# Optimization experiments

Hardware: AMD Instinct MI355X
Metric: run time of the kernel (lower is better)

The kernel has to match this reference:

```python
import jax, jax.numpy as jnp
import numpy as np

N = 100000
E = 1600000
IN, HID, OUT = 128, 256, 128


def setup_inputs() -> dict:
    key = jax.random.key(0)
    ks = jax.random.split(key, 8)
    x = jax.random.normal(ks[0], (N, IN), dtype=jnp.float32)
    edge_index = jax.random.randint(ks[1], (2, E), 0, N, dtype=jnp.int64)
    # PyG SAGEConv params: lin_l (neighbor aggr, with bias), lin_r (root, no bias)
    def glorot(k, shape):
        fan_in = shape[1]
        return jax.random.normal(k, shape, dtype=jnp.float32) / jnp.sqrt(jnp.float32(fan_in))
    W1l = glorot(ks[2], (HID, IN)); b1 = jnp.zeros((HID,), jnp.float32)
    W1r = glorot(ks[3], (HID, IN))
    W2l = glorot(ks[4], (OUT, HID)); b2 = jnp.zeros((OUT,), jnp.float32)
    W2r = glorot(ks[5], (OUT, HID))
    return {"x": x, "edge_index": edge_index, "W1l": W1l, "b1": b1,
            "W1r": W1r, "W2l": W2l, "b2": b2, "W2r": W2r}


def sage_conv(x, row, col, Wl, b, Wr, n_nodes):
    # mean-aggregate neighbor features x[row] at target nodes col
    msg = x[row]                                               # [E, d]
    s = jax.ops.segment_sum(msg, col, num_segments=n_nodes)    # [N, d]
    deg = jax.ops.segment_sum(jnp.ones((row.shape[0], 1), x.dtype), col,
                              num_segments=n_nodes)            # [N, 1]
    mean = s / jnp.maximum(deg, 1.0)
    return mean @ Wl.T + b + x @ Wr.T


def reference(x, edge_index, W1l, b1, W1r, W2l, b2, W2r):
    row, col = edge_index[0], edge_index[1]
    h = sage_conv(x, row, col, W1l, b1, W1r, N)
    h = jax.nn.relu(h)
    # dropout is identity in eval mode
    out = sage_conv(h, row, col, W2l, b2, W2r, N)
    return out
```

## Files before the change

kernel.cpp:

```cpp
#include <hip/hip_runtime.h>
#include <hip/hip_bf16.h>

#define NN 100000
#define NE 1600000
#define NCHUNK ((NN + 127) / 128)
#define NPB 512
#define NB 256
#define CHUNK 8192
#define NCH ((NE + CHUNK - 1) / CHUNK)

typedef __attribute__((ext_vector_type(8))) short short8;
typedef __attribute__((ext_vector_type(4))) float float4v;

__device__ __forceinline__ unsigned short f2bf(float f) {
    unsigned int b = __float_as_uint(f);
    return (unsigned short)((b + 0x7fffu + ((b >> 16) & 1u)) >> 16);
}
__device__ __forceinline__ unsigned int pack_bf16(float lo, float hi) {
    return (unsigned int)f2bf(lo) | ((unsigned int)f2bf(hi) << 16);
}
__device__ __forceinline__ float bflo(unsigned int u) { return __uint_as_float(u << 16); }
__device__ __forceinline__ float bfhi(unsigned int u) { return __uint_as_float(u & 0xffff0000u); }

__device__ __forceinline__ void addp(float* a, uint4 u) {
    a[0] += bflo(u.x); a[1] += bfhi(u.x);
    a[2] += bflo(u.y); a[3] += bfhi(u.y);
    a[4] += bflo(u.z); a[5] += bfhi(u.z);
    a[6] += bflo(u.w); a[7] += bfhi(u.w);
}

__global__ void k_wconv(const float* W1l, const float* W1r, const float* W2l, const float* W2r,
                        unsigned short* wb1, unsigned short* wb2) {
    int i = blockIdx.x * 256 + threadIdx.x;
    int r1 = i >> 7, c1 = i & 127;
    wb1[r1 * 256 + c1]       = f2bf(W1l[i]);
    wb1[r1 * 256 + 128 + c1] = f2bf(W1r[i]);
    wb2[i]         = f2bf(W2l[i]);
    wb2[32768 + i] = f2bf(W2r[i]);
}

__global__ void k_xconv(const float* x, unsigned int* axb_u) {
    int t = blockIdx.x * 256 + threadIdx.x;
    int node = t >> 6, i = t & 63;
    float2 v = ((const float2*)x)[t];
    axb_u[(size_t)node * 128 + 64 + i] = pack_bf16(v.x, v.y);
}

__global__ void k_bcount(const int* ei, int* bcnt) {
    __shared__ int h[NB];
    int t = threadIdx.x;
    h[t] = 0;
    __syncthreads();
    for (int e = blockIdx.x * 256 + t; e < NE; e += gridDim.x * 256)
        atomicAdd(&h[ei[NE + e] >> 9], 1);
    __syncthreads();
    if (h[t]) atomicAdd(&bcnt[t], h[t]);
}

__global__ void k_bscan(const int* bcnt, int* boff, int* bcur) {
    __shared__ int s[NB];
    int t = threadIdx.x;
    int v = bcnt[t];
    s[t] = v;
    __syncthreads();
    for (int d = 1; d < NB; d <<= 1) {
        int val = (t >= d) ? s[t - d] : 0;
        __syncthreads();
        s[t] += val;
        __syncthreads();
    }
    boff[t + 1] = s[t];
    if (t == 0) boff[0] = 0;
    bcur[t] = s[t] - v;
}

__global__ __launch_bounds__(256) void k_bscatter(const int* ei, int* bcur, uint2* pairs) {
    __shared__ uint2 buf[CHUNK];
    __shared__ int cnt[NB];
    __shared__ int lbase[NB];
    __shared__ int lcur[NB];
    __shared__ int gpos[NB];
    int t = threadIdx.x;
    int e0 = blockIdx.x * CHUNK;
    int nedge = NE - e0; if (nedge > CHUNK) nedge = CHUNK;
    cnt[t] = 0;
    __syncthreads();
    for (int i = t; i < nedge; i += 256)
        atomicAdd(&cnt[ei[NE + e0 + i] >> 9], 1);
    __syncthreads();
    int v = cnt[t];
    lcur[t] = v;
    __syncthreads();
    for (int d = 1; d < NB; d <<= 1) {
        int val = (t >= d) ? lcur[t - d] : 0;
        __syncthreads();
        lcur[t] += val;
        __syncthreads();
    }
    lbase[t] = lcur[t] - v;
    gpos[t] = atomicAdd(&bcur[t], v);
    __syncthreads();
    lcur[t] = lbase[t];
    __syncthreads();
    for (int i = t; i < nedge; i += 256) {
        int r = ei[e0 + i], c = ei[NE + e0 + i];
        int b = c >> 9;
        int p = atomicAdd(&lcur[b], 1);
        buf[p] = make_uint2((unsigned)r, (unsigned)c);
    }
    __syncthreads();
    int n = cnt[t], lb = lbase[t], gp = gpos[t];
    for (int i = 0; i < n; i++)
        pairs[gp + i] = buf[lb + i];
}

__global__ __launch_bounds__(256) void k_build(const uint2* pairs, const int* boff,
                                               int* off, int* deg, int* csr) {
    __shared__ int ldeg[NPB];
    __shared__ int lcur[NPB];
    __shared__ int sscan[256];
    int b = blockIdx.x;
    int nbase = b * NPB;
    if (nbase >= NN) return;
    int t = threadIdx.x;
    int base = boff[b], cntb = boff[b + 1] - base;
    ldeg[t] = 0; ldeg[t + 256] = 0;
    __syncthreads();
    for (int i = t; i < cntb; i += 256) {
        uint2 pr = pairs[base + i];
        atomicAdd(&ldeg[pr.y - nbase], 1);
    }
    __syncthreads();
    int d0 = ldeg[2 * t], d1 = ldeg[2 * t + 1];
    int v = d0 + d1;
    sscan[t] = v;
    __syncthreads();
    for (int d = 1; d < 256; d <<= 1) {
        int val = (t >= d) ? sscan[t - d] : 0;
        __syncthreads();
        sscan[t] += val;
        __syncthreads();
    }
    int ex = sscan[t] - v;
    lcur[2 * t] = ex; lcur[2 * t + 1] = ex + d0;
    __syncthreads();
    int nloc = NN - nbase; if (nloc > NPB) nloc = NPB;
    for (int ln = t; ln < nloc; ln += 256) {
        off[nbase + ln] = base + lcur[ln];
        deg[nbase + ln] = ldeg[ln];
    }
    __syncthreads();
    for (int i = t; i < cntb; i += 256) {
        uint2 pr = pairs[base + i];
        int p = atomicAdd(&lcur[pr.y - nbase], 1);
        csr[base + p] = (int)pr.x;
    }
}

__global__ void k_agg1(const unsigned int* axb_u, const int* off, const int* deg,
                       const int* csr, unsigned int* axb_w) {
    int wid = (blockIdx.x * 256 + threadIdx.x) >> 6;
    if (wid >= NN) return;
    int lane = threadIdx.x & 63;
    int sub = lane >> 4, l16 = lane & 15;
    int start = off[wid], d = deg[wid];
    float a[8] = {0.f, 0.f, 0.f, 0.f, 0.f, 0.f, 0.f, 0.f};
    int j = sub;
    for (; j + 4 < d; j += 8) {
        int nb0 = csr[start + j];
        int nb1 = csr[start + j + 4];
        uint4 u0 = *(const uint4*)(axb_u + (size_t)nb0 * 128 + 64 + (l16 << 2));
        uint4 u1 = *(const uint4*)(axb_u + (size_t)nb1 * 128 + 64 + (l16 << 2));
        addp(a, u0); addp(a, u1);
    }
    if (j < d) {
        int nb = csr[start + j];
        uint4 u = *(const uint4*)(axb_u + (size_t)nb * 128 + 64 + (l16 << 2));
        addp(a, u);
    }
#pragma unroll
    for (int i = 0; i < 8; i++) {
        a[i] += __shfl_xor(a[i], 16, 64);
        a[i] += __shfl_xor(a[i], 32, 64);
    }
    if (sub == 0) {
        float inv = 1.0f / (float)(d > 0 ? d : 1);
        uint4 o;
        o.x = pack_bf16(a[0] * inv, a[1] * inv);
        o.y = pack_bf16(a[2] * inv, a[3] * inv);
        o.z = pack_bf16(a[4] * inv, a[5] * inv);
        o.w = pack_bf16(a[6] * inv, a[7] * inv);
        *(uint4*)(axb_w + (size_t)wid * 128 + (l16 << 2)) = o;
    }
}

__global__ void k_agg2(const unsigned int* g, const int* off, const int* deg,
                       const int* csr, float* out) {
    int wid = (blockIdx.x * 256 + threadIdx.x) >> 6;
    if (wid >= NN) return;
    int lane = threadIdx.x & 63;
    int sub = lane >> 4, l16 = lane & 15;
    int start = off[wid], d = deg[wid];
    float a[8] = {0.f, 0.f, 0.f, 0.f, 0.f, 0.f, 0.f, 0.f};
    int j = sub;
    for (; j + 4 < d; j += 8) {
        int nb0 = csr[start + j];
        int nb1 = csr[start + j + 4];
        uint4 u0 = *(const uint4*)(g + (size_t)nb0 * 64 + (l16 << 2));
        uint4 u1 = *(const uint4*)(g + (size_t)nb1 * 64 + (l16 << 2));
        addp(a, u0); addp(a, u1);
    }
    if (j < d) {
        int nb = csr[start + j];
        uint4 u = *(const uint4*)(g + (size_t)nb * 64 + (l16 << 2));
        addp(a, u);
    }
#pragma unroll
    for (int i = 0; i < 8; i++) {
        a[i] += __shfl_xor(a[i], 16, 64);
        a[i] += __shfl_xor(a[i], 32, 64);
    }
    if (sub == 0) {
        float inv = 1.0f / (float)(d > 0 ? d : 1);
        float4* po = (float4*)(out + (size_t)wid * 128) + (l16 << 1);
        float4 c0 = po[0], c1 = po[1];
        c0.x += a[0] * inv; c0.y += a[1] * inv; c0.z += a[2] * inv; c0.w += a[3] * inv;
        c1.x += a[4] * inv; c1.y += a[5] * inv; c1.z += a[6] * inv; c1.w += a[7] * inv;
        po[0] = c0; po[1] = c1;
    }
}

__global__ __launch_bounds__(256, 1) void k_gemm1(const unsigned short* A, const unsigned short* wb,
                                                  const float* b1, unsigned short* H) {
    __shared__ unsigned short Bs[256 * 256];
    int t = threadIdx.x;
    {
        const short8* src = (const short8*)wb;
        short8* dst = (short8*)Bs;
#pragma unroll
        for (int i = 0; i < 32; i++) dst[i * 256 + t] = src[i * 256 + t];
    }
    __syncthreads();
    int wv = t >> 6, lane = t & 63;
    int mrow = lane & 15, quad = lane >> 4;
    float bias[16];
#pragma unroll
    for (int ct = 0; ct < 16; ct++) bias[ct] = b1[ct * 16 + mrow];
    for (int chunk = blockIdx.x; chunk < NCHUNK; chunk += gridDim.x) {
        int base = chunk * 128 + wv * 32;
        if (base >= NN) continue;
        short8 afr[2][8];
#pragma unroll
        for (int kk = 0; kk < 8; kk++) {
            afr[0][kk] = *(const short8*)(A + (size_t)(base + mrow) * 256 + kk * 32 + quad * 8);
            afr[1][kk] = *(const short8*)(A + (size_t)(base + 16 + mrow) * 256 + kk * 32 + quad * 8);
        }
        float4v acc[2][16];
#pragma unroll
        for (int h = 0; h < 2; h++)
#pragma unroll
            for (int ct = 0; ct < 16; ct++) acc[h][ct] = (float4v)(0.0f);
#pragma unroll
        for (int kk = 0; kk < 8; kk++) {
            int koff = kk * 32 + quad * 8;
#pragma unroll
            for (int ct = 0; ct < 16; ct++) {
                short8 b = *(const short8*)(Bs + (ct * 16 + mrow) * 256 + koff);
                acc[0][ct] = __builtin_amdgcn_mfma_f32_16x16x32_bf16(afr[0][kk], b, acc[0][ct], 0, 0, 0);
                acc[1][ct] = __builtin_amdgcn_mfma_f32_16x16x32_bf16(afr[1][kk], b, acc[1][ct], 0, 0, 0);
            }
        }
#pragma unroll
        for (int ct = 0; ct < 16; ct++) {
            int col = ct * 16 + mrow;
#pragma unroll
            for (int h = 0; h < 2; h++) {
#pragma unroll
                for (int r = 0; r < 4; r++) {
                    int node = base + h * 16 + quad * 4 + r;
                    float v = acc[h][ct][r] + bias[ct];
                    v = fmaxf(v, 0.f);
                    H[(size_t)node * 256 + col] = f2bf(v);
                }
            }
        }
    }
}

__global__ __launch_bounds__(256, 1) void k_gemm2(const unsigned short* A, const unsigned short* wb,
                                                  const float* b2, unsigned short* g, float* out) {
    __shared__ unsigned short Bs[256 * 256];
    int t = threadIdx.x;
    {
        const short8* src = (const short8*)wb;
        short8* dst = (short8*)Bs;
#pragma unroll
        for (int i = 0; i < 32; i++) dst[i * 256 + t] = src[i * 256 + t];
    }
    __syncthreads();
    int wv = t >> 6, lane = t & 63;
    int mrow = lane & 15, quad = lane >> 4;
    float bias[8];
#pragma unroll
    for (int i = 0; i < 8; i++) bias[i] = b2[i * 16 + mrow];
    for (int chunk = blockIdx.x; chunk < NCHUNK; chunk += gridDim.x) {
        int base = chunk * 128 + wv * 32;
        if (base >= NN) continue;
        short8 afr[2][8];
#pragma unroll
        for (int kk = 0; kk < 8; kk++) {
            afr[0][kk] = *(const short8*)(A + (size_t)(base + mrow) * 256 + kk * 32 + quad * 8);
            afr[1][kk] = *(const short8*)(A + (size_t)(base + 16 + mrow) * 256 + kk * 32 + quad * 8);
        }
        float4v acc[2][16];
#pragma unroll
        for (int h = 0; h < 2; h++)
#pragma unroll
            for (int ct = 0; ct < 16; ct++) acc[h][ct] = (float4v)(0.0f);
#pragma unroll
        for (int kk = 0; kk < 8; kk++) {
            int koff = kk * 32 + quad * 8;
#pragma unroll
            for (int ct = 0; ct < 16; ct++) {
                short8 b = *(const short8*)(Bs + (ct * 16 + mrow) * 256 + koff);
                acc[0][ct] = __builtin_amdgcn_mfma_f32_16x16x32_bf16(afr[0][kk], b, acc[0][ct], 0, 0, 0);
                acc[1][ct] = __builtin_amdgcn_mfma_f32_16x16x32_bf16(afr[1][kk], b, acc[1][ct], 0, 0, 0);
            }
        }
#pragma unroll
        for (int ct = 0; ct < 16; ct++) {
            int col = ct * 16 + mrow;
#pragma unroll
            for (int h = 0; h < 2; h++) {
#pragma unroll
                for (int r = 0; r < 4; r++) {
                    int node = base + h * 16 + quad * 4 + r;
                    float v = acc[h][ct][r];
                    if (ct < 8) {
                        g[(size_t)node * 128 + col] = f2bf(v);
                    } else {
                        out[(size_t)node * 128 + (col - 128)] = v + bias[ct - 8];
                    }
                }
            }
        }
    }
}

extern "C" void kernel_launch(void* const* d_in, const int* in_sizes, int n_in,
                              void* d_out, int out_size, void* d_ws, size_t ws_size,
                              hipStream_t stream) {
    const float* x   = (const float*)d_in[0];
    const int*   ei  = (const int*)d_in[1];
    const float* W1l = (const float*)d_in[2];
    const float* b1  = (const float*)d_in[3];
    const float* W1r = (const float*)d_in[4];
    const float* W2l = (const float*)d_in[5];
    const float* b2  = (const float*)d_in[6];
    const float* W2r = (const float*)d_in[7];
    float* out = (float*)d_out;

    char* p = (char*)d_ws;
    unsigned int* axb = (unsigned int*)p; p += (size_t)NN * 256 * 2;
    unsigned short* h = (unsigned short*)p; p += (size_t)NN * 256 * 2;
    unsigned int* g   = (unsigned int*)p;  p += (size_t)NN * 128 * 2;
    unsigned short* wb1 = (unsigned short*)p; p += 65536 * 2;
    unsigned short* wb2 = (unsigned short*)p; p += 65536 * 2;
    int* deg  = (int*)p; p += (size_t)NN * 4;
    int* off  = (int*)p; p += (size_t)NN * 4;
    int* csr  = (int*)p; p += (size_t)NE * 4;
    int* bcnt = (int*)p; p += NB * 4;
    int* boff = (int*)p; p += (NB + 1) * 4;
    int* bcur = (int*)p; p += NB * 4;
    if (ws_size < (size_t)(p - (char*)d_ws)) return;
    uint2* pairs = (uint2*)h;

    hipMemsetAsync(bcnt, 0, NB * 4, stream);
    k_wconv<<<128, 256, 0, stream>>>(W1l, W1r, W2l, W2r, wb1, wb2);
    k_xconv<<<NN * 64 / 256, 256, 0, stream>>>(x, axb);
    k_bcount<<<256, 256, 0, stream>>>(ei, bcnt);
    k_bscan<<<1, NB, 0, stream>>>(bcnt, boff, bcur);
    k_bscatter<<<NCH, 256, 0, stream>>>(ei, bcur, pairs);
    k_build<<<NB, 256, 0, stream>>>(pairs, boff, off, deg, csr);
    k_agg1<<<NN * 64 / 256, 256, 0, stream>>>(axb, off, deg, csr, axb);
    k_gemm1<<<256, 256, 0, stream>>>((const unsigned short*)axb, wb1, b1, h);
    k_gemm2<<<256, 256, 0, stream>>>(h, wb2, b2, (unsigned short*)g, out);
    k_agg2<<<25000, 256, 0, stream>>>(g, off, deg, csr, out);
}
```

Baseline: 396.5 us.

## Merge prep kernels, unroll gather loops, and double-buffer A fragments in GEMMs

Merges the weight conversion, x conversion and bucket-count kernels into one launch that splits work by block index, which removes two launches. Widens the neighbor-gather loops in both aggregation kernels to keep four loads in flight per lane group. Makes both GEMM kernels prefetch the next chunk's A fragments into a second register buffer while the current chunk runs its MFMAs. The extra buffer doubles A-fragment register use and may add spills, and the bcount edge partition of 256×6250 relies on E being exactly 1.6M.

After: 410.4 us. 1.03x slower.

```diff
diff --git a/kernel.cpp b/kernel.cpp
--- a/kernel.cpp
+++ b/kernel.cpp
@@ -29,32 +29,33 @@
     a[6] += bflo(u.w); a[7] += bfhi(u.w);
 }
 
-__global__ void k_wconv(const float* W1l, const float* W1r, const float* W2l, const float* W2r,
-                        unsigned short* wb1, unsigned short* wb2) {
-    int i = blockIdx.x * 256 + threadIdx.x;
-    int r1 = i >> 7, c1 = i & 127;
-    wb1[r1 * 256 + c1]       = f2bf(W1l[i]);
-    wb1[r1 * 256 + 128 + c1] = f2bf(W1r[i]);
-    wb2[i]         = f2bf(W2l[i]);
-    wb2[32768 + i] = f2bf(W2r[i]);
-}
-
-__global__ void k_xconv(const float* x, unsigned int* axb_u) {
-    int t = blockIdx.x * 256 + threadIdx.x;
-    int node = t >> 6, i = t & 63;
-    float2 v = ((const float2*)x)[t];
-    axb_u[(size_t)node * 128 + 64 + i] = pack_bf16(v.x, v.y);
-}
-
-__global__ void k_bcount(const int* ei, int* bcnt) {
-    __shared__ int h[NB];
-    int t = threadIdx.x;
-    h[t] = 0;
-    __syncthreads();
-    for (int e = blockIdx.x * 256 + t; e < NE; e += gridDim.x * 256)
-        atomicAdd(&h[ei[NE + e] >> 9], 1);
-    __syncthreads();
-    if (h[t]) atomicAdd(&bcnt[t], h[t]);
+__global__ void k_prep(const float* x, const float* W1l, const float* W1r,
+                       const float* W2l, const float* W2r, const int* ei,
+                       unsigned int* axb_u, unsigned short* wb1, unsigned short* wb2,
+                       int* bcnt) {
+    __shared__ int hh[NB];
+    int b = blockIdx.x, t = threadIdx.x;
+    if (b < 25000) {
+        int tt = b * 256 + t;
+        int node = tt >> 6, i = tt & 63;
+        float2 v = ((const float2*)x)[tt];
+        axb_u[(size_t)node * 128 + 64 + i] = pack_bf16(v.x, v.y);
+    } else if (b < 25128) {
+        int i = (b - 25000) * 256 + t;
+        int r1 = i >> 7, c1 = i & 127;
+        wb1[r1 * 256 + c1]       = f2bf(W1l[i]);
+        wb1[r1 * 256 + 128 + c1] = f2bf(W1r[i]);
+        wb2[i]         = f2bf(W2l[i]);
+        wb2[32768 + i] = f2bf(W2r[i]);
+    } else {
+        hh[t] = 0;
+        __syncthreads();
+        int e0 = (b - 25128) * 6250;
+        for (int e = e0 + t; e < e0 + 6250; e += 256)
+            atomicAdd(&hh[ei[NE + e] >> 9], 1);
+        __syncthreads();
+        if (hh[t]) atomicAdd(&bcnt[t], hh[t]);
+    }
 }
 
 __global__ void k_bscan(const int* bcnt, int* boff, int* bcur) {
@@ -164,18 +165,23 @@
     int lane = threadIdx.x & 63;
     int sub = lane >> 4, l16 = lane & 15;
     int start = off[wid], d = deg[wid];
+    const unsigned int* gp = axb_u + 64 + (l16 << 2);
     float a[8] = {0.f, 0.f, 0.f, 0.f, 0.f, 0.f, 0.f, 0.f};
     int j = sub;
-    for (; j + 4 < d; j += 8) {
-        int nb0 = csr[start + j];
-        int nb1 = csr[start + j + 4];
-        uint4 u0 = *(const uint4*)(axb_u + (size_t)nb0 * 128 + 64 + (l16 << 2));
-        uint4 u1 = *(const uint4*)(axb_u + (size_t)nb1 * 128 + 64 + (l16 << 2));
-        addp(a, u0); addp(a, u1);
-    }
-    if (j < d) {
+    for (; j + 12 < d; j += 16) {
+        int n0 = csr[start + j];
+        int n1 = csr[start + j + 4];
+        int n2 = csr[start + j + 8];
+        int n3 = csr[start + j + 12];
+        uint4 u0 = *(const uint4*)(gp + (size_t)n0 * 128);
+        uint4 u1 = *(const uint4*)(gp + (size_t)n1 * 128);
+        uint4 u2 = *(const uint4*)(gp + (size_t)n2 * 128);
+        uint4 u3 = *(const uint4*)(gp + (size_t)n3 * 128);
+        addp(a, u0); addp(a, u1); addp(a, u2); addp(a, u3);
+    }
+    for (; j < d; j += 4) {
         int nb = csr[start + j];
-        uint4 u = *(const uint4*)(axb_u + (size_t)nb * 128 + 64 + (l16 << 2));
+        uint4 u = *(const uint4*)(gp + (size_t)nb * 128);
         addp(a, u);
     }
 #pragma unroll
@@ -201,18 +207,23 @@
     int lane = threadIdx.x & 63;
     int sub = lane >> 4, l16 = lane & 15;
     int start = off[wid], d = deg[wid];
+    const unsigned int* gp = g + (l16 << 2);
     float a[8] = {0.f, 0.f, 0.f, 0.f, 0.f, 0.f, 0.f, 0.f};
     int j = sub;
-    for (; j + 4 < d; j += 8) {
-        int nb0 = csr[start + j];
-        int nb1 = csr[start + j + 4];
-        uint4 u0 = *(const uint4*)(g + (size_t)nb0 * 64 + (l16 << 2));
-        uint4 u1 = *(const uint4*)(g + (size_t)nb1 * 64 + (l16 << 2));
-        addp(a, u0); addp(a, u1);
-    }
-    if (j < d) {
+    for (; j + 12 < d; j += 16) {
+        int n0 = csr[start + j];
+        int n1 = csr[start + j + 4];
+        int n2 = csr[start + j + 8];
+        int n3 = csr[start + j + 12];
+        uint4 u0 = *(const uint4*)(gp + (size_t)n0 * 64);
+        uint4 u1 = *(const uint4*)(gp + (size_t)n1 * 64);
+        uint4 u2 = *(const uint4*)(gp + (size_t)n2 * 64);
+        uint4 u3 = *(const uint4*)(gp + (size_t)n3 * 64);
+        addp(a, u0); addp(a, u1); addp(a, u2); addp(a, u3);
+    }
+    for (; j < d; j += 4) {
         int nb = csr[start + j];
-        uint4 u = *(const uint4*)(g + (size_t)nb * 64 + (l16 << 2));
+        uint4 u = *(const uint4*)(gp + (size_t)nb * 64);
         addp(a, u);
     }
 #pragma unroll
@@ -230,6 +241,32 @@
     }
 }
 
+__device__ __forceinline__ void loadA(short8 afr[2][8], const unsigned short* A,
+                                      int base, int mrow, int quad) {
+#pragma unroll
+    for (int kk = 0; kk < 8; kk++) {
+        afr[0][kk] = *(const short8*)(A + (size_t)(base + mrow) * 256 + kk * 32 + quad * 8);
+        afr[1][kk] = *(const short8*)(A + (size_t)(base + 16 + mrow) * 256 + kk * 32 + quad * 8);
+    }
+}
+__device__ __forceinline__ void mfmaAcc(float4v acc[2][16], short8 afr[2][8],
+                                        const unsigned short* Bs, int mrow, int quad) {
+#pragma unroll
+    for (int h = 0; h < 2; h++)
+#pragma unroll
+        for (int ct = 0; ct < 16; ct++) acc[h][ct] = (float4v)(0.0f);
+#pragma unroll
+    for (int kk = 0; kk < 8; kk++) {
+        int koff = kk * 32 + quad * 8;
+#pragma unroll
+        for (int ct = 0; ct < 16; ct++) {
+            short8 b = *(const short8*)(Bs + (ct * 16 + mrow) * 256 + koff);
+            acc[0][ct] = __builtin_amdgcn_mfma_f32_16x16x32_bf16(afr[0][kk], b, acc[0][ct], 0, 0, 0);
+            acc[1][ct] = __builtin_amdgcn_mfma_f32_16x16x32_bf16(afr[1][kk], b, acc[1][ct], 0, 0, 0);
+        }
+    }
+}
+
 __global__ __launch_bounds__(256, 1) void k_gemm1(const unsigned short* A, const unsigned short* wb,
                                                   const float* b1, unsigned short* H) {
     __shared__ unsigned short Bs[256 * 256];
@@ -240,50 +277,41 @@
 #pragma unroll
         for (int i = 0; i < 32; i++) dst[i * 256 + t] = src[i * 256 + t];
     }
-    __syncthreads();
     int wv = t >> 6, lane = t & 63;
     int mrow = lane & 15, quad = lane >> 4;
     float bias[16];
 #pragma unroll
     for (int ct = 0; ct < 16; ct++) bias[ct] = b1[ct * 16 + mrow];
-    for (int chunk = blockIdx.x; chunk < NCHUNK; chunk += gridDim.x) {
-        int base = chunk * 128 + wv * 32;
-        if (base >= NN) continue;
-        short8 afr[2][8];
-#pragma unroll
-        for (int kk = 0; kk < 8; kk++) {
-            afr[0][kk] = *(const short8*)(A + (size_t)(base + mrow) * 256 + kk * 32 + quad * 8);
-            afr[1][kk] = *(const short8*)(A + (size_t)(base + 16 + mrow) * 256 + kk * 32 + quad * 8);
+    short8 afrA[2][8], afrB[2][8];
+    int chunk = blockIdx.x;
+    int base = chunk * 128 + wv * 32;
+    if (base < NN) loadA(afrA, A, base, mrow, quad);
+    __syncthreads();
+    bool useA = true;
+    while (chunk < NCHUNK) {
+        int cn = chunk + 256;
+        int bn = cn * 128 + wv * 32;
+        if (cn < NCHUNK && bn < NN) {
+            if (useA) loadA(afrB, A, bn, mrow, quad);
+            else      loadA(afrA, A, bn, mrow, quad);
         }
-        float4v acc[2][16];
-#pragma unroll
-        for (int h = 0; h < 2; h++)
-#pragma unroll
-            for (int ct = 0; ct < 16; ct++) acc[h][ct] = (float4v)(0.0f);
-#pragma unroll
-        for (int kk = 0; kk < 8; kk++) {
-            int koff = kk * 32 + quad * 8;
+        if (base < NN) {
+            float4v acc[2][16];
+            mfmaAcc(acc, useA ? afrA : afrB, Bs, mrow, quad);
 #pragma unroll
             for (int ct = 0; ct < 16; ct++) {
-                short8 b = *(const short8*)(Bs + (ct * 16 + mrow) * 256 + koff);
-                acc[0][ct] = __builtin_amdgcn_mfma_f32_16x16x32_bf16(afr[0][kk], b, acc[0][ct], 0, 0, 0);
-                acc[1][ct] = __builtin_amdgcn_mfma_f32_16x16x32_bf16(afr[1][kk], b, acc[1][ct], 0, 0, 0);
+                int col = ct * 16 + mrow;
+#pragma unroll
+                for (int h = 0; h < 2; h++)
+#pragma unroll
+                    for (int r = 0; r < 4; r++) {
+                        int node = base + h * 16 + quad * 4 + r;
+                        float v = acc[h][ct][r] + bias[ct];
+                        H[(size_t)node * 256 + col] = f2bf(fmaxf(v, 0.f));
+                    }
             }
         }
-#pragma unroll
-        for (int ct = 0; ct < 16; ct++) {
-            int col = ct * 16 + mrow;
-#pragma unroll
-            for (int h = 0; h < 2; h++) {
-#pragma unroll
-                for (int r = 0; r < 4; r++) {
-                    int node = base + h * 16 + quad * 4 + r;
-                    float v = acc[h][ct][r] + bias[ct];
-                    v = fmaxf(v, 0.f);
-                    H[(size_t)node * 256 + col] = f2bf(v);
-                }
-            }
-        }
+        chunk = cn; base = bn; useA = !useA;
     }
 }
 
@@ -297,53 +325,42 @@
 #pragma unroll
         for (int i = 0; i < 32; i++) dst[i * 256 + t] = src[i * 256 + t];
     }
-    __syncthreads();
     int wv = t >> 6, lane = t & 63;
     int mrow = lane & 15, quad = lane >> 4;
     float bias[8];
 #pragma unroll
     for (int i = 0; i < 8; i++) bias[i] = b2[i * 16 + mrow];
-    for (int chunk = blockIdx.x; chunk < NCHUNK; chunk += gridDim.x) {
-        int base = chunk * 128 + wv * 32;
-        if (base >= NN) continue;
-        short8 afr[2][8];
-#pragma unroll
-        for (int kk = 0; kk < 8; kk++) {
-            afr[0][kk] = *(const short8*)(A + (size_t)(base + mrow) * 256 + kk * 32 + quad * 8);
-            afr[1][kk] = *(const short8*)(A + (size_t)(base + 16 + mrow) * 256 + kk * 32 + quad * 8);
+    short8 afrA[2][8], afrB[2][8];
+    int chunk = blockIdx.x;
+    int base = chunk * 128 + wv * 32;
+    if (base < NN) loadA(afrA, A, base, mrow, quad);
+    __syncthreads();
+    bool useA = true;
+    while (chunk < NCHUNK) {
+        int cn = chunk + 256;
+        int bn = cn * 128 + wv * 32;
+        if (cn < NCHUNK && bn < NN) {
+            if (useA) loadA(afrB, A, bn, mrow, quad);
+            else      loadA(afrA, A, bn, mrow, quad);
         }
-        float4v acc[2][16];
-#pragma unroll
-        for (int h = 0; h < 2; h++)
-#pragma unroll
-            for (int ct = 0; ct < 16; ct++) acc[h][ct] = (float4v)(0.0f);
-#pragma unroll
-        for (int kk = 0; kk < 8; kk++) {
-            int koff = kk * 32 + quad * 8;
+        if (base < NN) {
+            float4v acc[2][16];
+            mfmaAcc(acc, useA ? afrA : afrB, Bs, mrow, quad);
 #pragma unroll
             for (int ct = 0; ct < 16; ct++) {
-                short8 b = *(const short8*)(Bs + (ct * 16 + mrow) * 256 + koff);
-                acc[0][ct] = __builtin_amdgcn_mfma_f32_16x16x32_bf16(afr[0][kk], b, acc[0][ct], 0, 0, 0);
-                acc[1][ct] = __builtin_amdgcn_mfma_f32_16x16x32_bf16(afr[1][kk], b, acc[1][ct], 0, 0, 0);
+                int col = ct * 16 + mrow;
+#pragma unroll
+                for (int h = 0; h < 2; h++)
+#pragma unroll
+                    for (int r = 0; r < 4; r++) {
+                        int node = base + h * 16 + quad * 4 + r;
+                        float v = acc[h][ct][r];
+                        if (ct < 8) g[(size_t)node * 128 + col] = f2bf(v);
+                        else        out[(size_t)node * 128 + (col - 128)] = v + bias[ct - 8];
+                    }
             }
         }
-#pragma unroll
-        for (int ct = 0; ct < 16; ct++) {
-            int col = ct * 16 + mrow;
-#pragma unroll
-            for (int h = 0; h < 2; h++) {
-#pragma unroll
-                for (int r = 0; r < 4; r++) {
-                    int node = base + h * 16 + quad * 4 + r;
-                    float v = acc[h][ct][r];
-                    if (ct < 8) {
-                        g[(size_t)node * 128 + col] = f2bf(v);
-                    } else {
-                        out[(size_t)node * 128 + (col - 128)] = v + bias[ct - 8];
-                    }
-                }
-            }
-        }
+        chunk = cn; base = bn; useA = !useA;
     }
 }
 
@@ -376,9 +393,7 @@
     uint2* pairs = (uint2*)h;
 
     hipMemsetAsync(bcnt, 0, NB * 4, stream);
-    k_wconv<<<128, 256, 0, stream>>>(W1l, W1r, W2l, W2r, wb1, wb2);
-    k_xconv<<<NN * 64 / 256, 256, 0, stream>>>(x, axb);
-    k_bcount<<<256, 256, 0, stream>>>(ei, bcnt);
+    k_prep<<<25384, 256, 0, stream>>>(x, W1l, W1r, W2l, W2r, ei, axb, wb1, wb2, bcnt);
     k_bscan<<<1, NB, 0, stream>>>(bcnt, boff, bcur);
     k_bscatter<<<NCH, 256, 0, stream>>>(ei, bcur, pairs);
     k_build<<<NB, 256, 0, stream>>>(pairs, boff, off, deg, csr);
```

## Store layer-2 transformed features in FP8, fuse prep kernels, parallelize bucket copy

Applied to the files above, without the earlier changes.

The layer-2 message tensor g is now stored as FP8 instead of BF16, which halves the bytes gathered per edge in the second aggregation; it is decoded with the packed fp8-to-f32 conversion builtin. The weight conversion, x conversion and bucket-count kernels are merged into one launch. The per-bucket copy in the scatter kernel now uses wave-strided parallel writes instead of one thread serially copying each bucket. FP8 storage cuts gather bandwidth but loses precision in the layer-2 messages, which may push the output past tolerance.

New measurement: 375.3 us. 5.3% less time.

```diff
diff --git a/kernel.cpp b/kernel.cpp
--- a/kernel.cpp
+++ b/kernel.cpp
@@ -11,6 +11,7 @@
 
 typedef __attribute__((ext_vector_type(8))) short short8;
 typedef __attribute__((ext_vector_type(4))) float float4v;
+typedef __attribute__((ext_vector_type(2))) float float2v;
 
 __device__ __forceinline__ unsigned short f2bf(float f) {
     unsigned int b = __float_as_uint(f);
@@ -28,33 +29,45 @@
     a[4] += bflo(u.z); a[5] += bfhi(u.z);
     a[6] += bflo(u.w); a[7] += bfhi(u.w);
 }
-
-__global__ void k_wconv(const float* W1l, const float* W1r, const float* W2l, const float* W2r,
-                        unsigned short* wb1, unsigned short* wb2) {
-    int i = blockIdx.x * 256 + threadIdx.x;
-    int r1 = i >> 7, c1 = i & 127;
-    wb1[r1 * 256 + c1]       = f2bf(W1l[i]);
-    wb1[r1 * 256 + 128 + c1] = f2bf(W1r[i]);
-    wb2[i]         = f2bf(W2l[i]);
-    wb2[32768 + i] = f2bf(W2r[i]);
-}
-
-__global__ void k_xconv(const float* x, unsigned int* axb_u) {
-    int t = blockIdx.x * 256 + threadIdx.x;
-    int node = t >> 6, i = t & 63;
-    float2 v = ((const float2*)x)[t];
-    axb_u[(size_t)node * 128 + 64 + i] = pack_bf16(v.x, v.y);
-}
-
-__global__ void k_bcount(const int* ei, int* bcnt) {
-    __shared__ int h[NB];
-    int t = threadIdx.x;
-    h[t] = 0;
-    __syncthreads();
-    for (int e = blockIdx.x * 256 + t; e < NE; e += gridDim.x * 256)
-        atomicAdd(&h[ei[NE + e] >> 9], 1);
-    __syncthreads();
-    if (h[t]) atomicAdd(&bcnt[t], h[t]);
+__device__ __forceinline__ void addp8(float* a, uint2 u) {
+    float2v f;
+    f = __builtin_amdgcn_cvt_pk_f32_fp8(u.x, false); a[0] += f.x; a[1] += f.y;
+    f = __builtin_amdgcn_cvt_pk_f32_fp8(u.x, true);  a[2] += f.x; a[3] += f.y;
+    f = __builtin_amdgcn_cvt_pk_f32_fp8(u.y, false); a[4] += f.x; a[5] += f.y;
+    f = __builtin_amdgcn_cvt_pk_f32_fp8(u.y, true);  a[6] += f.x; a[7] += f.y;
+}
+__device__ __forceinline__ unsigned char f2fp8(float v) {
+    int r = __builtin_amdgcn_cvt_pk_fp8_f32(v, v, 0, false);
+    return (unsigned char)(r & 0xff);
+}
+
+__global__ void k_prep(const float* x, const float* W1l, const float* W1r,
+                       const float* W2l, const float* W2r, const int* ei,
+                       unsigned int* axb_u, unsigned short* wb1, unsigned short* wb2,
+                       int* bcnt) {
+    __shared__ int hh[NB];
+    int b = blockIdx.x, t = threadIdx.x;
+    if (b < 25000) {
+        int tt = b * 256 + t;
+        int node = tt >> 6, i = tt & 63;
+        float2 v = ((const float2*)x)[tt];
+        axb_u[(size_t)node * 128 + 64 + i] = pack_bf16(v.x, v.y);
+    } else if (b < 25128) {
+        int i = (b - 25000) * 256 + t;
+        int r1 = i >> 7, c1 = i & 127;
+        wb1[r1 * 256 + c1]       = f2bf(W1l[i]);
+        wb1[r1 * 256 + 128 + c1] = f2bf(W1r[i]);
+        wb2[i]         = f2bf(W2l[i]);
+        wb2[32768 + i] = f2bf(W2r[i]);
+    } else {
+        hh[t] = 0;
+        __syncthreads();
+        int e0 = (b - 25128) * 6250;
+        for (int e = e0 + t; e < e0 + 6250; e += 256)
+            atomicAdd(&hh[ei[NE + e] >> 9], 1);
+        __syncthreads();
+        if (hh[t]) atomicAdd(&bcnt[t], hh[t]);
+    }
 }
 
 __global__ void k_bscan(const int* bcnt, int* boff, int* bcur) {
@@ -109,9 +122,12 @@
         buf[p] = make_uint2((unsigned)r, (unsigned)c);
     }
     __syncthreads();
-    int n = cnt[t], lb = lbase[t], gp = gpos[t];
-    for (int i = 0; i < n; i++)
-        pairs[gp + i] = buf[lb + i];
+    int wv = t >> 6, lane = t & 63;
+    for (int b = wv; b < NB; b += 4) {
+        int n = cnt[b], lb = lbase[b], gp = gpos[b];
+        for (int i = lane; i < n; i += 64)
+            pairs[gp + i] = buf[lb + i];
+    }
 }
 
 __global__ __launch_bounds__(256) void k_build(const uint2* pairs, const int* boff,
@@ -164,18 +180,19 @@
     int lane = threadIdx.x & 63;
     int sub = lane >> 4, l16 = lane & 15;
     int start = off[wid], d = deg[wid];
+    const unsigned int* gp = axb_u + 64 + (l16 << 2);
     float a[8] = {0.f, 0.f, 0.f, 0.f, 0.f, 0.f, 0.f, 0.f};
     int j = sub;
     for (; j + 4 < d; j += 8) {
-        int nb0 = csr[start + j];
-        int nb1 = csr[start + j + 4];
-        uint4 u0 = *(const uint4*)(axb_u + (size_t)nb0 * 128 + 64 + (l16 << 2));
-        uint4 u1 = *(const uint4*)(axb_u + (size_t)nb1 * 128 + 64 + (l16 << 2));
+        int n0 = csr[start + j];
+        int n1 = csr[start + j + 4];
+        uint4 u0 = *(const uint4*)(gp + (size_t)n0 * 128);
+        uint4 u1 = *(const uint4*)(gp + (size_t)n1 * 128);
         addp(a, u0); addp(a, u1);
     }
     if (j < d) {
         int nb = csr[start + j];
-        uint4 u = *(const uint4*)(axb_u + (size_t)nb * 128 + 64 + (l16 << 2));
+        uint4 u = *(const uint4*)(gp + (size_t)nb * 128);
         addp(a, u);
     }
 #pragma unroll
@@ -194,26 +211,27 @@
     }
 }
 
-__global__ void k_agg2(const unsigned int* g, const int* off, const int* deg,
+__global__ void k_agg2(const uint2* g, const int* off, const int* deg,
                        const int* csr, float* out) {
     int wid = (blockIdx.x * 256 + threadIdx.x) >> 6;
     if (wid >= NN) return;
     int lane = threadIdx.x & 63;
     int sub = lane >> 4, l16 = lane & 15;
     int start = off[wid], d = deg[wid];
+    const uint2* gp = g + l16;
     float a[8] = {0.f, 0.f, 0.f, 0.f, 0.f, 0.f, 0.f, 0.f};
     int j = sub;
     for (; j + 4 < d; j += 8) {
-        int nb0 = csr[start + j];
-        int nb1 = csr[start + j + 4];
-        uint4 u0 = *(const uint4*)(g + (size_t)nb0 * 64 + (l16 << 2));
-        uint4 u1 = *(const uint4*)(g + (size_t)nb1 * 64 + (l16 << 2));
-        addp(a, u0); addp(a, u1);
+        int n0 = csr[start + j];
+        int n1 = csr[start + j + 4];
+        uint2 u0 = gp[(size_t)n0 * 16];
+        uint2 u1 = gp[(size_t)n1 * 16];
+        addp8(a, u0); addp8(a, u1);
     }
     if (j < d) {
         int nb = csr[start + j];
-        uint4 u = *(const uint4*)(g + (size_t)nb * 64 + (l16 << 2));
-        addp(a, u);
+        uint2 u = gp[(size_t)nb * 16];
+        addp8(a, u);
     }
 #pragma unroll
     for (int i = 0; i < 8; i++) {
@@ -274,21 +292,19 @@
         for (int ct = 0; ct < 16; ct++) {
             int col = ct * 16 + mrow;
 #pragma unroll
-            for (int h = 0; h < 2; h++) {
+            for (int h = 0; h < 2; h++)
 #pragma unroll
                 for (int r = 0; r < 4; r++) {
                     int node = base + h * 16 + quad * 4 + r;
                     float v = acc[h][ct][r] + bias[ct];
-                    v = fmaxf(v, 0.f);
-                    H[(size_t)node * 256 + col] = f2bf(v);
+                    H[(size_t)node * 256 + col] = f2bf(fmaxf(v, 0.f));
                 }
-            }
         }
     }
 }
 
 __global__ __launch_bounds__(256, 1) void k_gemm2(const unsigned short* A, const unsigned short* wb,
-                                                  const float* b2, unsigned short* g, float* out) {
+                                                  const float* b2, unsigned char* g, float* out) {
     __shared__ unsigned short Bs[256 * 256];
     int t = threadIdx.x;
     {
@@ -331,18 +347,14 @@
         for (int ct = 0; ct < 16; ct++) {
             int col = ct * 16 + mrow;
 #pragma unroll
-            for (int h = 0; h < 2; h++) {
+            for (int h = 0; h < 2; h++)
 #pragma unroll
                 for (int r = 0; r < 4; r++) {
                     int node = base + h * 16 + quad * 4 + r;
                     float v = acc[h][ct][r];
-                    if (ct < 8) {
-                        g[(size_t)node * 128 + col] = f2bf(v);
-                    } else {
-                        out[(size_t)node * 128 + (col - 128)] = v + bias[ct - 8];
-                    }
+                    if (ct < 8) g[(size_t)node * 128 + col] = f2fp8(v);
+                    else        out[(size_t)node * 128 + (col - 128)] = v + bias[ct - 8];
                 }
-            }
         }
     }
 }
@@ -363,7 +375,7 @@
     char* p = (char*)d_ws;
     unsigned int* axb = (unsigned int*)p; p += (size_t)NN * 256 * 2;
     unsigned short* h = (unsigned short*)p; p += (size_t)NN * 256 * 2;
-    unsigned int* g   = (unsigned int*)p;  p += (size_t)NN * 128 * 2;
+    unsigned char* g  = (unsigned char*)p; p += (size_t)NN * 128;
     unsigned short* wb1 = (unsigned short*)p; p += 65536 * 2;
     unsigned short* wb2 = (unsigned short*)p; p += 65536 * 2;
     int* deg  = (int*)p; p += (size_t)NN * 4;
@@ -376,14 +388,12 @@
     uint2* pairs = (uint2*)h;
 
     hipMemsetAsync(bcnt, 0, NB * 4, stream);
-    k_wconv<<<128, 256, 0, stream>>>(W1l, W1r, W2l, W2r, wb1, wb2);
-    k_xconv<<<NN * 64 / 256, 256, 0, stream>>>(x, axb);
-    k_bcount<<<256, 256, 0, stream>>>(ei, bcnt);
+    k_prep<<<25384, 256, 0, stream>>>(x, W1l, W1r, W2l, W2r, ei, axb, wb1, wb2, bcnt);
     k_bscan<<<1, NB, 0, stream>>>(bcnt, boff, bcur);
     k_bscatter<<<NCH, 256, 0, stream>>>(ei, bcur, pairs);
     k_build<<<NB, 256, 0, stream>>>(pairs, boff, off, deg, csr);
     k_agg1<<<NN * 64 / 256, 256, 0, stream>>>(axb, off, deg, csr, axb);
     k_gemm1<<<256, 256, 0, stream>>>((const unsigned short*)axb, wb1, b1, h);
-    k_gemm2<<<256, 256, 0, stream>>>(h, wb2, b2, (unsigned short*)g, out);
-    k_agg2<<<25000, 256, 0, stream>>>(g, off, deg, csr, out);
-}
+    k_gemm2<<<256, 256, 0, stream>>>(h, wb2, b2, g, out);
+    k_agg2<<<25000, 256, 0, stream>>>((const uint2*)g, off, deg, csr, out);
+}
```
